# Kernel tuning notes

Hardware: AMD Instinct MI355X
Metric: run time of the kernel (lower is better)

The kernel has to match this reference:

```python
import jax, jax.numpy as jnp
import numpy as np
from jax import lax

# init kwargs (hardcoded per module config)
T_D = 0.3            # condensation radius
T_B = 0.85           # min beta threshold
FEATURE_LENGTH = 9   # x[:, FEATURE_LENGTH:] are predictions
N_TOT_FEAT = 17      # => n_ccoords = 17 - 14 = 3
MAX_COND = 1024      # static pad size for the boolean-mask gather output

B = 4
S = 250000
N = B * S


def setup_inputs() -> dict:
    key = jax.random.key(0)
    kx, = jax.random.split(key, 1)
    x = jax.random.uniform(kx, (N, N_TOT_FEAT), dtype=jnp.float32)  # betas in [0,1)
    row_splits = jnp.arange(B + 1, dtype=jnp.int32) * S             # equal ragged splits
    return {"x": x, "row_splits": row_splits}


def _condense(x, n_seg, seg_len):
    """Greedy BuildCondensates (hard/soft=False): per segment, repeatedly pick the
    unassigned point of max beta (>= T_B), assign all unassigned points within
    radius T_D of it in cluster-coordinate space, until no candidate remains."""
    n_ccoords = x.shape[-1] - 14
    x_pred = x[:, FEATURE_LENGTH:]
    betas = x_pred[:, 0].reshape(n_seg, seg_len)                     # (B,S)
    cc = x_pred[:, x_pred.shape[-1] - n_ccoords:].reshape(n_seg, seg_len, n_ccoords)
    col = jnp.arange(seg_len, dtype=jnp.int32)[None, :]              # (1,S)

    asso0 = -jnp.ones((n_seg, seg_len), jnp.int32)
    iscond0 = jnp.zeros((n_seg, seg_len), jnp.int32)

    def body(state):
        asso, iscond, _ = state
        unassigned = asso < 0
        score = jnp.where(unassigned, betas, -jnp.inf)
        max_idx = jnp.argmax(score, axis=1).astype(jnp.int32)        # (B,) per-segment argmax beta
        max_beta = jnp.take_along_axis(score, max_idx[:, None], axis=1)[:, 0]
        found = max_beta >= T_B                                      # (B,)
        c = jnp.take_along_axis(cc, max_idx[:, None, None], axis=1)  # (B,1,nc)
        distsq = jnp.sum((cc - c) ** 2, axis=-1)                     # (B,S)
        assign = unassigned & (distsq < T_D * T_D) & found[:, None]
        asso = jnp.where(assign, max_idx[:, None], asso)
        iscond = jnp.where(assign & (col == max_idx[:, None]), 1, iscond)
        return (asso, iscond, jnp.any(found))

    asso, iscond, _ = lax.while_loop(lambda s: s[2], body,
                                     (asso0, iscond0, jnp.array(True)))
    ncond_per_seg = jnp.sum(iscond, axis=1, dtype=jnp.int32)         # (B,)
    # output row splits for condensates: [0, cumsum...]
    ncond = jnp.concatenate([jnp.zeros((1,), jnp.int32),
                             jnp.cumsum(ncond_per_seg).astype(jnp.int32)])
    return asso, iscond.reshape(-1), ncond


def reference(x, row_splits):
    n_seg = row_splits.shape[0] - 1          # static
    seg_len = x.shape[0] // n_seg            # equal splits assumed (matches setup)
    _, iscond, ncond = _condense(x, n_seg, seg_len)
    # boolean-mask gather dout = x[iscond > 0], padded to static MAX_COND rows
    idx = jnp.nonzero(iscond > 0, size=MAX_COND, fill_value=0)[0]
    total = jnp.sum(iscond)
    valid = (jnp.arange(MAX_COND) < total).astype(x.dtype)           # (K,)
    dout = x[idx] * valid[:, None]                                   # (K, F), zero-padded
    return dout, ncond
```

## Files before the change

### kernel.cpp

```cpp
#include <hip/hip_runtime.h>
#include <stdint.h>

typedef unsigned long long u64;
typedef unsigned int u32;
typedef unsigned char u8;


#define DSQ(ax,ay,az,bx,by,bz) \
    __fadd_rn(__fadd_rn(__fmul_rn(__fsub_rn(ax,bx),__fsub_rn(ax,bx)), \
                        __fmul_rn(__fsub_rn(ay,by),__fsub_rn(ay,by))), \
              __fmul_rn(__fsub_rn(az,bz),__fsub_rn(az,bz)))

#define INS5(k, cx, cy, cz) do { u64 _k = (k); \
    if (_k > K5) { \
      if (_k > K4) { K5 = K4; \
        if (_k > K3) { K4 = K3; X4=X3; Y4=Y3; Z4=Z3; \
          if (_k > K2) { K3 = K2; X3=X2; Y3=Y2; Z3=Z2; \
            if (_k > K1) { K2 = K1; X2=X1; Y2=Y1; Z2=Z1; \
                           K1 = _k; X1=(cx); Y1=(cy); Z1=(cz); } \
            else { K2 = _k; X2=(cx); Y2=(cy); Z2=(cz); } } \
          else { K3 = _k; X3=(cx); Y3=(cy); Z3=(cz); } } \
        else { K4 = _k; X4=(cx); Y4=(cy); Z4=(cz); } } \
      else K5 = _k; \
    } } while (0)

__global__ void init_kernel(int* segCount, int* condTotal, int* scanned,
                            int* doneF, int* aliveCnt, int nseg) {
    int t = threadIdx.x;
    if (t < nseg) {
        segCount[t] = 0; condTotal[t] = 0; scanned[t] = 0;
        doneF[t] = 0; aliveCnt[t] = 0;
    }
}

__launch_bounds__(256)
__global__ void filter_scan0(const float* __restrict__ x, int S, int chunk, int bps,
                             int* __restrict__ segCount,
                             float4* __restrict__ A, int* __restrict__ iA,
                             u8* __restrict__ aliveB, int CAP,
                             u64* __restrict__ btK, float4* __restrict__ btC) {
    __shared__ float4 stg[1024];
    __shared__ int sgi[1024];
    __shared__ int s_cnt, s_base;
    __shared__ u64 mK[4][5];
    __shared__ float mC[4][12];
    const int b = blockIdx.x;
    const int s = b / bps, c = b % bps;
    const int tid = threadIdx.x, lane = tid & 63, wid = tid >> 6;
    int start = s * S + c * chunk;
    int end = min(start + chunk, s * S + S);
    if (tid == 0) s_cnt = 0;
    __syncthreads();
    for (int i = start + tid; i < end; i += 256) {
        float beta = x[(size_t)i * 17 + 9];
        if (beta >= 0.85f) {
            int p = atomicAdd(&s_cnt, 1);
            if (p < 1024) {
                stg[p] = make_float4(x[(size_t)i * 17 + 14], x[(size_t)i * 17 + 15],
                                     x[(size_t)i * 17 + 16], beta);
                sgi[p] = i;
            }
        }
    }
    __syncthreads();
    if (tid == 0) s_base = atomicAdd(&segCount[s], min(s_cnt, 1024));
    __syncthreads();
    int cnt = min(s_cnt, 1024);

    u64 K1=0,K2=0,K3=0,K4=0,K5=0;
    float X1=0,Y1=0,Z1=0,X2=0,Y2=0,Z2=0,X3=0,Y3=0,Z3=0,X4=0,Y4=0,Z4=0;
    for (int k = tid; k < cnt; k += 256) {
        int pos = s_base + k;
        float4 cd = stg[k];
        int gi = sgi[k];
        if (pos < CAP) {
            A[(size_t)s * CAP + pos] = cd;
            iA[(size_t)s * CAP + pos] = gi;
            aliveB[(size_t)s * CAP + pos] = 1;
            u64 key = ((u64)__float_as_uint(cd.w) << 32) | (u64)(~(u32)gi);
            INS5(key, cd.x, cd.y, cd.z);
        }
    }
    for (int off = 32; off > 0; off >>= 1) {
        u64 o1=__shfl_xor(K1,off), o2=__shfl_xor(K2,off), o3=__shfl_xor(K3,off),
            o4=__shfl_xor(K4,off), o5=__shfl_xor(K5,off);
        float a1=__shfl_xor(X1,off), b1=__shfl_xor(Y1,off), c1=__shfl_xor(Z1,off);
        float a2=__shfl_xor(X2,off), b2=__shfl_xor(Y2,off), c2=__shfl_xor(Z2,off);
        float a3=__shfl_xor(X3,off), b3=__shfl_xor(Y3,off), c3=__shfl_xor(Z3,off);
        float a4=__shfl_xor(X4,off), b4=__shfl_xor(Y4,off), c4=__shfl_xor(Z4,off);
        INS5(o1,a1,b1,c1); INS5(o2,a2,b2,c2); INS5(o3,a3,b3,c3); INS5(o4,a4,b4,c4);
        if (o5 > K5) K5 = o5;
    }
    if (lane == 0) {
        mK[wid][0]=K1; mK[wid][1]=K2; mK[wid][2]=K3; mK[wid][3]=K4; mK[wid][4]=K5;
        mC[wid][0]=X1; mC[wid][1]=Y1; mC[wid][2]=Z1; mC[wid][3]=X2; mC[wid][4]=Y2;
        mC[wid][5]=Z2; mC[wid][6]=X3; mC[wid][7]=Y3; mC[wid][8]=Z3; mC[wid][9]=X4;
        mC[wid][10]=Y4; mC[wid][11]=Z4;
    }
    __syncthreads();
    if (tid == 0) {
        for (int w = 1; w < 4; ++w) {
            INS5(mK[w][0], mC[w][0], mC[w][1], mC[w][2]);
            INS5(mK[w][1], mC[w][3], mC[w][4], mC[w][5]);
            INS5(mK[w][2], mC[w][6], mC[w][7], mC[w][8]);
            INS5(mK[w][3], mC[w][9], mC[w][10], mC[w][11]);
            if (mK[w][4] > K5) K5 = mK[w][4];
        }
        btK[(size_t)b*5+0]=K1; btK[(size_t)b*5+1]=K2; btK[(size_t)b*5+2]=K3;
        btK[(size_t)b*5+3]=K4; btK[(size_t)b*5+4]=K5;
        btC[(size_t)b*4+0]=make_float4(X1,Y1,Z1,0.f);
        btC[(size_t)b*4+1]=make_float4(X2,Y2,Z2,0.f);
        btC[(size_t)b*4+2]=make_float4(X3,Y3,Z3,0.f);
        btC[(size_t)b*4+3]=make_float4(X4,Y4,Z4,0.f);
    }
}

__launch_bounds__(256)
__global__ void scan_r(const float4* __restrict__ A, const int* __restrict__ iA,
                       const int* __restrict__ segCount, int CAP,
                       const float4* __restrict__ gctr,
                       const int* __restrict__ condTotal, const int* __restrict__ scanned,
                       const int* __restrict__ doneF, u8* __restrict__ aliveB,
                       u64* __restrict__ btK, float4* __restrict__ btC,
                       int* __restrict__ aliveCnt) {
    const int b = blockIdx.x;
    const int s = b >> 8, c = b & 255;
    const int tid = threadIdx.x, lane = tid & 63, wid = tid >> 6;
    __shared__ float4 ctrL[1024];
    __shared__ u64 mK[4][5];
    __shared__ float mC[4][12];
    __shared__ int wAl[4];
    if (doneF[s]) return;

    int n = segCount[s]; if (n > CAP) n = CAP;
    const int c0 = scanned[s], c1 = condTotal[s];
    const int nc = c1 - c0;
    for (int i = tid; i < nc; i += 256) ctrL[i] = gctr[(size_t)s * 1024 + c0 + i];
    __syncthreads();

    const int chunkC = (n + 255) >> 8;
    const int j0 = c * chunkC;
    const int j1 = min(j0 + chunkC, n);

    u64 K1=0,K2=0,K3=0,K4=0,K5=0;
    float X1=0,Y1=0,Z1=0,X2=0,Y2=0,Z2=0,X3=0,Y3=0,Z3=0,X4=0,Y4=0,Z4=0;
    int myAlive = 0;
    for (int j = j0 + tid; j < j1; j += 256) {
        if (!aliveB[(size_t)s * CAP + j]) continue;
        float4 cd = A[(size_t)s * CAP + j];
        bool live = true;
        for (int m = 0; m < nc; ++m) {
            float4 q = ctrL[m];
            if (DSQ(cd.x, cd.y, cd.z, q.x, q.y, q.z) < 0.09f) { live = false; break; }
        }
        if (!live) { aliveB[(size_t)s * CAP + j] = 0; continue; }
        ++myAlive;
        u64 key = ((u64)__float_as_uint(cd.w) << 32) | (u64)(~(u32)iA[(size_t)s * CAP + j]);
        INS5(key, cd.x, cd.y, cd.z);
    }
    for (int off = 32; off > 0; off >>= 1) {
        u64 o1=__shfl_xor(K1,off), o2=__shfl_xor(K2,off), o3=__shfl_xor(K3,off),
            o4=__shfl_xor(K4,off), o5=__shfl_xor(K5,off);
        float a1=__shfl_xor(X1,off), b1=__shfl_xor(Y1,off), c1v=__shfl_xor(Z1,off);
        float a2=__shfl_xor(X2,off), b2=__shfl_xor(Y2,off), c2v=__shfl_xor(Z2,off);
        float a3=__shfl_xor(X3,off), b3=__shfl_xor(Y3,off), c3v=__shfl_xor(Z3,off);
        float a4=__shfl_xor(X4,off), b4=__shfl_xor(Y4,off), c4v=__shfl_xor(Z4,off);
        INS5(o1,a1,b1,c1v); INS5(o2,a2,b2,c2v); INS5(o3,a3,b3,c3v); INS5(o4,a4,b4,c4v);
        if (o5 > K5) K5 = o5;
        myAlive += __shfl_xor(myAlive, off);
    }
    if (lane == 0) {
        mK[wid][0]=K1; mK[wid][1]=K2; mK[wid][2]=K3; mK[wid][3]=K4; mK[wid][4]=K5;
        mC[wid][0]=X1; mC[wid][1]=Y1; mC[wid][2]=Z1; mC[wid][3]=X2; mC[wid][4]=Y2;
        mC[wid][5]=Z2; mC[wid][6]=X3; mC[wid][7]=Y3; mC[wid][8]=Z3; mC[wid][9]=X4;
        mC[wid][10]=Y4; mC[wid][11]=Z4;
        wAl[wid] = myAlive;
    }
    __syncthreads();
    if (tid == 0) {
        for (int w = 1; w < 4; ++w) {
            INS5(mK[w][0], mC[w][0], mC[w][1], mC[w][2]);
            INS5(mK[w][1], mC[w][3], mC[w][4], mC[w][5]);
            INS5(mK[w][2], mC[w][6], mC[w][7], mC[w][8]);
            INS5(mK[w][3], mC[w][9], mC[w][10], mC[w][11]);
            if (mK[w][4] > K5) K5 = mK[w][4];
        }
        btK[(size_t)b*5+0]=K1; btK[(size_t)b*5+1]=K2; btK[(size_t)b*5+2]=K3;
        btK[(size_t)b*5+3]=K4; btK[(size_t)b*5+4]=K5;
        btC[(size_t)b*4+0]=make_float4(X1,Y1,Z1,0.f);
        btC[(size_t)b*4+1]=make_float4(X2,Y2,Z2,0.f);
        btC[(size_t)b*4+2]=make_float4(X3,Y3,Z3,0.f);
        btC[(size_t)b*4+3]=make_float4(X4,Y4,Z4,0.f);
        int tot = wAl[0] + wAl[1] + wAl[2] + wAl[3];
        if (tot) atomicAdd(&aliveCnt[s], tot);
    }
}

__launch_bounds__(64)
__global__ void pop_k(const u64* __restrict__ btK, const float4* __restrict__ btC,
                      float4* __restrict__ gctr, int* __restrict__ gctrGi,
                      int* __restrict__ condTotal, int* __restrict__ scanned,
                      int* __restrict__ doneF, int* __restrict__ aliveCnt, int check) {
    const int s = blockIdx.x, lane = threadIdx.x;
    if (doneF[s]) return;
    if (check && aliveCnt[s] == 0) { if (lane == 0) doneF[s] = 1; return; }

    u64 k[16]; float4 c[16];
    u64 h = 0;
    #pragma unroll
    for (int q = 0; q < 16; ++q) {
        int bb = (s << 8) + (lane << 2) + (q >> 2);
        int slot = q & 3;
        k[q] = btK[(size_t)bb * 5 + slot];
        c[q] = btC[(size_t)bb * 4 + slot];
        if ((q & 3) == 0) {
            u64 k5 = btK[(size_t)bb * 5 + 4];
            if (k5 > h) h = k5;
        }
    }
    for (int off = 32; off > 0; off >>= 1) {
        u64 o = __shfl_xor(h, off);
        if (o > h) h = o;
    }
    const u64 H = h;

    int ct = condTotal[s];
    const int start = ct;
    while (ct < 1024) {
        u64 mk = k[0]; float4 mc = c[0];
        #pragma unroll
        for (int q = 1; q < 16; ++q)
            if (k[q] > mk) { mk = k[q]; mc = c[q]; }
        for (int off = 32; off > 0; off >>= 1) {
            u64 ok = __shfl_xor(mk, off);
            float ox = __shfl_xor(mc.x, off);
            float oy = __shfl_xor(mc.y, off);
            float oz = __shfl_xor(mc.z, off);
            if (ok > mk) { mk = ok; mc.x = ox; mc.y = oy; mc.z = oz; }
        }
        if (mk <= H) break;
        #pragma unroll
        for (int q = 0; q < 16; ++q)
            if (k[q] && DSQ(c[q].x, c[q].y, c[q].z, mc.x, mc.y, mc.z) < 0.09f) k[q] = 0;
        if (lane == 0) {
            gctr[(size_t)s * 1024 + ct] = make_float4(mc.x, mc.y, mc.z, 0.f);
            gctrGi[(size_t)s * 1024 + ct] = (int)(~(u32)(mk & 0xFFFFFFFFull));
        }
        ct++;
    }
    if (lane == 0) { scanned[s] = start; condTotal[s] = ct; aliveCnt[s] = 0; }
}

__launch_bounds__(1024)
__global__ void fallback_k(const float4* __restrict__ A, const int* __restrict__ iA,
                           const int* __restrict__ segCount, int CAP,
                           const float4* __restrict__ gctr, int* __restrict__ gctrGi,
                           int* __restrict__ condTotalG, int* __restrict__ scannedG,
                           const int* __restrict__ doneF, u8* __restrict__ aliveB) {
    const int s = blockIdx.x, tid = threadIdx.x, lane = tid & 63, wid = tid >> 6;
    __shared__ float4 ctr[1024];
    __shared__ int ctrGi[1024];
    __shared__ u64 wk[2][16];
    __shared__ float4 wc[2][16];
    __shared__ u64 s_H;
    __shared__ int s_alive;
    if (doneF[s]) return;

    const float4* cand = A + (size_t)s * CAP;
    const int* gia = iA + (size_t)s * CAP;
    u8* alv = aliveB + (size_t)s * CAP;
    int n = segCount[s]; if (n > CAP) n = CAP;
    int condTotal = condTotalG[s];
    int scanned = scannedG[s];
    for (int i = tid; i < condTotal; i += 1024) {
        ctr[i] = gctr[(size_t)s * 1024 + i];
        ctrGi[i] = gctrGi[(size_t)s * 1024 + i];
    }
    int passes = 0, par = 0;
    __syncthreads();

    while (true) {
        if (tid == 0) { s_H = 0; s_alive = 0; }
        __syncthreads();
        u64 k1 = 0, k2 = 0, k3 = 0;
        float4 C1 = make_float4(0,0,0,0), C2 = make_float4(0,0,0,0);
        int myAlive = 0;
        for (int j = tid; j < n; j += 1024) {
            if (!alv[j]) continue;
            float4 c = cand[j];
            bool live = true;
            for (int m = scanned; m < condTotal; ++m) {
                float4 q = ctr[m];
                if (DSQ(c.x, c.y, c.z, q.x, q.y, q.z) < 0.09f) { live = false; break; }
            }
            if (!live) { alv[j] = 0; continue; }
            ++myAlive;
            u64 key = ((u64)__float_as_uint(c.w) << 32) | (u64)(~(u32)gia[j]);
            if (key > k1)      { k3 = k2; k2 = k1; C2 = C1; k1 = key; C1 = c; }
            else if (key > k2) { k3 = k2; k2 = key; C2 = c; }
            else if (key > k3) { k3 = key; }
        }
        int asum = myAlive; u64 h = k3;
        for (int off = 32; off > 0; off >>= 1) {
            asum += __shfl_down(asum, off);
            u64 o = __shfl_down(h, off);
            if (o > h) h = o;
        }
        if (lane == 0) { atomicAdd(&s_alive, asum); atomicMax(&s_H, h); }
        __syncthreads();
        if (s_alive == 0) break;
        u64 H = s_H;
        scanned = condTotal;
        while (condTotal < 1024) {
            u64 mk; float4 bc;
            if (k1 >= k2) { mk = k1; bc = C1; } else { mk = k2; bc = C2; }
            for (int off = 32; off > 0; off >>= 1) {
                u64 ok = __shfl_xor(mk, off);
                float ox = __shfl_xor(bc.x, off);
                float oy = __shfl_xor(bc.y, off);
                float oz = __shfl_xor(bc.z, off);
                if (ok > mk) { mk = ok; bc.x = ox; bc.y = oy; bc.z = oz; }
            }
            if (lane == 0) { wk[par][wid] = mk; wc[par][wid] = bc; }
            __syncthreads();
            u64 bk = 0; int bL = 0;
            #pragma unroll
            for (int w = 0; w < 16; ++w) {
                u64 kk = wk[par][w];
                if (kk > bk) { bk = kk; bL = w; }
            }
            if (bk <= H) break;
            float4 cc = wc[par][bL];
            if (k1 && DSQ(C1.x, C1.y, C1.z, cc.x, cc.y, cc.z) < 0.09f) k1 = 0;
            if (k2 && DSQ(C2.x, C2.y, C2.z, cc.x, cc.y, cc.z) < 0.09f) k2 = 0;
            if (tid == 0) { ctr[condTotal] = cc; ctrGi[condTotal] = (int)(~(u32)(bk & 0xFFFFFFFFull)); }
            condTotal++;
            par ^= 1;
        }
        __syncthreads();
        if (condTotal >= 1024 || ++passes > 128) break;
    }

    for (int i = tid; i < condTotal; i += 1024)
        gctrGi[(size_t)s * 1024 + i] = ctrGi[i];
    if (tid == 0) condTotalG[s] = condTotal;
}

__global__ void finalize_kernel(const int* __restrict__ ctrGi,
                                const int* __restrict__ condTotal,
                                int* __restrict__ sorted, int* __restrict__ prefix,
                                float* __restrict__ ncond_out, int nseg, int rows) {
    __shared__ int lst[1024];
    __shared__ int pfx[9];
    int tid = threadIdx.x;
    if (tid == 0) {
        int acc = 0; pfx[0] = 0;
        for (int s2 = 0; s2 < nseg; s2++) { acc += condTotal[s2]; pfx[s2 + 1] = acc; }
    }
    __syncthreads();
    if (tid <= nseg) { prefix[tid] = pfx[tid]; ncond_out[tid] = (float)pfx[tid]; }
    for (int s2 = 0; s2 < nseg; s2++) {
        int ns = condTotal[s2]; if (ns > 1024) ns = 1024;
        for (int i = tid; i < ns; i += blockDim.x) lst[i] = ctrGi[(size_t)s2 * 1024 + i];
        __syncthreads();
        for (int i = tid; i < ns; i += blockDim.x) {
            int v = lst[i]; int rank = 0;
            for (int j = 0; j < ns; j++) rank += (lst[j] < v);
            int pos = pfx[s2] + rank;
            if (pos < rows) sorted[pos] = v;
        }
        __syncthreads();
    }
}

__global__ void emit_kernel(const float* __restrict__ x, const int* __restrict__ sorted,
                            const int* __restrict__ prefix, float* __restrict__ out,
                            int rows, int nseg) {
    int e = blockIdx.x * blockDim.x + threadIdx.x;
    if (e >= rows * 17) return;
    int total = prefix[nseg];
    int j = e / 17, k = e - j * 17;
    float v = 0.f;
    if (j < total) v = x[(size_t)sorted[j] * 17 + k];
    out[e] = v;
}

extern "C" void kernel_launch(void* const* d_in, const int* in_sizes, int n_in,
                              void* d_out, int out_size, void* d_ws, size_t ws_size,
                              hipStream_t stream) {
    const float* x = (const float*)d_in[0];
    const int nseg = in_sizes[1] - 1;
    const int N = in_sizes[0] / 17;
    const int S = N / nseg;
    const int rows = (out_size - (nseg + 1)) / 17;
    const int NROUNDS = 2;

    const int bps = 256;
    const int nBlocks = nseg * bps;
    const int chunk = (S + bps - 1) / bps;

    size_t fixedBytes = (size_t)nseg * 1024 * 16  +
                        (size_t)nBlocks * 4 * 16  +
                        (size_t)nBlocks * 5 * 8   +
                        (size_t)nseg * 1024 * 4   +
                        (size_t)nseg * 4 * 5  +
                        (size_t)rows * 4 + (size_t)(nseg + 1) * 4 + 8192;
    size_t perCand = (size_t)nseg * (16 + 4 + 1);
    size_t avail = (ws_size > fixedBytes) ? (ws_size - fixedBytes) : 0;
    int CAP = (int)(avail / perCand);
    if (CAP > 65536) CAP = 65536;
    if (CAP < 1) CAP = 1;

    char* w = (char*)d_ws;
    float4* A    = (float4*)w;                 w += (size_t)nseg * CAP * 16;
    float4* ctr  = (float4*)w;                 w += (size_t)nseg * 1024 * 16;
    float4* btC  = (float4*)w;                 w += (size_t)nBlocks * 4 * 16;
    u64* btK     = (u64*)w;                    w += (size_t)nBlocks * 5 * 8;
    int* iA      = (int*)w;                    w += (size_t)nseg * CAP * 4;
    int* ctrGi   = (int*)w;                    w += (size_t)nseg * 1024 * 4;
    int* segCount  = (int*)w;                  w += (size_t)nseg * 4;
    int* condTotal = (int*)w;                  w += (size_t)nseg * 4;
    int* scanned   = (int*)w;                  w += (size_t)nseg * 4;
    int* doneF     = (int*)w;                  w += (size_t)nseg * 4;
    int* aliveCnt  = (int*)w;                  w += (size_t)nseg * 4;
    int* sorted    = (int*)w;                  w += (size_t)rows * 4;
    int* prefix    = (int*)w;                  w += (size_t)(nseg + 1) * 4;
    u8* aliveB     = (u8*)w;
    float* out = (float*)d_out;

    init_kernel<<<1, 64, 0, stream>>>(segCount, condTotal, scanned, doneF,
                                      aliveCnt, nseg);
    filter_scan0<<<nBlocks, 256, 0, stream>>>(x, S, chunk, bps, segCount,
                                              A, iA, aliveB, CAP, btK, btC);
    pop_k<<<nseg, 64, 0, stream>>>(btK, btC, ctr, ctrGi, condTotal, scanned,
                                   doneF, aliveCnt, 0);
    for (int r = 0; r < NROUNDS; ++r) {
        scan_r<<<nBlocks, 256, 0, stream>>>(A, iA, segCount, CAP, ctr, condTotal,
                                            scanned, doneF, aliveB, btK, btC, aliveCnt);
        pop_k<<<nseg, 64, 0, stream>>>(btK, btC, ctr, ctrGi, condTotal, scanned,
                                       doneF, aliveCnt, 1);
    }
    fallback_k<<<nseg, 1024, 0, stream>>>(A, iA, segCount, CAP, ctr, ctrGi,
                                          condTotal, scanned, doneF, aliveB);
    finalize_kernel<<<1, 256, 0, stream>>>(ctrGi, condTotal, sorted, prefix,
                                           out + (size_t)rows * 17, nseg, rows);
    emit_kernel<<<(rows * 17 + 255) / 256, 256, 0, stream>>>(x, sorted, prefix, out,
                                                             rows, nseg);
}
```

Before: 165.6 us.

## Vectorize filter loads as float4 groups of four rows, shrink pop shuffles

The filter kernel now processes four consecutive 17-float rows per thread by loading only the needed float4 words, extracting betas and cluster coordinates for each row, and reserving staging slots with one shared atomic per thread. This replaces scalar strided loads and per-row atomics. The pop kernel's argmax reduction now shuffles a source-lane index instead of three coordinates, then broadcasts the winner once. The init kernel is replaced by a memset. The change assumes S is divisible by 4 and that the input base is 16-byte aligned; each block now covers one group per thread, which relies on chunkG being at most 256.

```diff
diff --git a/kernel.cpp b/kernel.cpp
--- a/kernel.cpp
+++ b/kernel.cpp
@@ -24,17 +24,8 @@
       else K5 = _k; \
     } } while (0)
 
-__global__ void init_kernel(int* segCount, int* condTotal, int* scanned,
-                            int* doneF, int* aliveCnt, int nseg) {
-    int t = threadIdx.x;
-    if (t < nseg) {
-        segCount[t] = 0; condTotal[t] = 0; scanned[t] = 0;
-        doneF[t] = 0; aliveCnt[t] = 0;
-    }
-}
-
 __launch_bounds__(256)
-__global__ void filter_scan0(const float* __restrict__ x, int S, int chunk, int bps,
+__global__ void filter_scan0(const float* __restrict__ x, int Sg, int chunkG, int bps,
                              int* __restrict__ segCount,
                              float4* __restrict__ A, int* __restrict__ iA,
                              u8* __restrict__ aliveB, int CAP,
@@ -47,21 +38,36 @@
     const int b = blockIdx.x;
     const int s = b / bps, c = b % bps;
     const int tid = threadIdx.x, lane = tid & 63, wid = tid >> 6;
-    int start = s * S + c * chunk;
-    int end = min(start + chunk, s * S + S);
+    const int segG0 = s * Sg;
+    const int g = segG0 + c * chunkG + tid;
+    const bool valid = (g < segG0 + Sg) && (tid < chunkG);
     if (tid == 0) s_cnt = 0;
     __syncthreads();
-    for (int i = start + tid; i < end; i += 256) {
-        float beta = x[(size_t)i * 17 + 9];
-        if (beta >= 0.85f) {
-            int p = atomicAdd(&s_cnt, 1);
-            if (p < 1024) {
-                stg[p] = make_float4(x[(size_t)i * 17 + 14], x[(size_t)i * 17 + 15],
-                                     x[(size_t)i * 17 + 16], beta);
-                sgi[p] = i;
-            }
-        }
-    }
+
+    float be0=0, be1=0, be2=0, be3=0;
+    float4 cc0, cc1, cc2, cc3;
+    int r0 = 0;
+    if (valid) {
+        const float4* p = (const float4*)x + (size_t)g * 17;
+        float4 v2 = p[2],  v3 = p[3],  v4 = p[4];
+        float4 v6 = p[6],  v7 = p[7],  v8 = p[8];
+        float4 v10 = p[10], v12 = p[12];
+        float4 v15 = p[15], v16 = p[16];
+        r0 = g * 4;
+        be0 = v2.y;  cc0 = make_float4(v3.z,  v3.w,  v4.x,  be0);
+        be1 = v6.z;  cc1 = make_float4(v7.w,  v8.x,  v8.y,  be1);
+        be2 = v10.w; cc2 = make_float4(v12.x, v12.y, v12.z, be2);
+        be3 = v15.x; cc3 = make_float4(v16.y, v16.z, v16.w, be3);
+    }
+    bool h0 = valid && (be0 >= 0.85f), h1 = valid && (be1 >= 0.85f);
+    bool h2 = valid && (be2 >= 0.85f), h3 = valid && (be3 >= 0.85f);
+    int nh = (h0?1:0) + (h1?1:0) + (h2?1:0) + (h3?1:0);
+    int p0 = 0;
+    if (nh) p0 = atomicAdd(&s_cnt, nh);
+    if (h0) { if (p0 < 1024) { stg[p0] = cc0; sgi[p0] = r0;     } p0++; }
+    if (h1) { if (p0 < 1024) { stg[p0] = cc1; sgi[p0] = r0 + 1; } p0++; }
+    if (h2) { if (p0 < 1024) { stg[p0] = cc2; sgi[p0] = r0 + 2; } p0++; }
+    if (h3) { if (p0 < 1024) { stg[p0] = cc3; sgi[p0] = r0 + 3; } p0++; }
     __syncthreads();
     if (tid == 0) s_base = atomicAdd(&segCount[s], min(s_cnt, 1024));
     __syncthreads();
@@ -231,19 +237,21 @@
         #pragma unroll
         for (int q = 1; q < 16; ++q)
             if (k[q] > mk) { mk = k[q]; mc = c[q]; }
+        int src = lane;
         for (int off = 32; off > 0; off >>= 1) {
             u64 ok = __shfl_xor(mk, off);
-            float ox = __shfl_xor(mc.x, off);
-            float oy = __shfl_xor(mc.y, off);
-            float oz = __shfl_xor(mc.z, off);
-            if (ok > mk) { mk = ok; mc.x = ox; mc.y = oy; mc.z = oz; }
+            int os = __shfl_xor(src, off);
+            if (ok > mk) { mk = ok; src = os; }
         }
         if (mk <= H) break;
+        float cx = __shfl(mc.x, src);
+        float cy = __shfl(mc.y, src);
+        float cz = __shfl(mc.z, src);
         #pragma unroll
         for (int q = 0; q < 16; ++q)
-            if (k[q] && DSQ(c[q].x, c[q].y, c[q].z, mc.x, mc.y, mc.z) < 0.09f) k[q] = 0;
+            if (k[q] && DSQ(c[q].x, c[q].y, c[q].z, cx, cy, cz) < 0.09f) k[q] = 0;
         if (lane == 0) {
-            gctr[(size_t)s * 1024 + ct] = make_float4(mc.x, mc.y, mc.z, 0.f);
+            gctr[(size_t)s * 1024 + ct] = make_float4(cx, cy, cz, 0.f);
             gctrGi[(size_t)s * 1024 + ct] = (int)(~(u32)(mk & 0xFFFFFFFFull));
         }
         ct++;
@@ -397,7 +405,8 @@
 
     const int bps = 256;
     const int nBlocks = nseg * bps;
-    const int chunk = (S + bps - 1) / bps;
+    const int Sg = S >> 2;
+    const int chunkG = (Sg + bps - 1) / bps;
 
     size_t fixedBytes = (size_t)nseg * 1024 * 16  +
                         (size_t)nBlocks * 4 * 16  +
@@ -428,9 +437,8 @@
     u8* aliveB     = (u8*)w;
     float* out = (float*)d_out;
 
-    init_kernel<<<1, 64, 0, stream>>>(segCount, condTotal, scanned, doneF,
-                                      aliveCnt, nseg);
-    filter_scan0<<<nBlocks, 256, 0, stream>>>(x, S, chunk, bps, segCount,
+    hipMemsetAsync(segCount, 0, (size_t)nseg * 5 * 4, stream);
+    filter_scan0<<<nBlocks, 256, 0, stream>>>(x, Sg, chunkG, bps, segCount,
                                               A, iA, aliveB, CAP, btK, btC);
     pop_k<<<nseg, 64, 0, stream>>>(btK, btC, ctr, ctrGi, condTotal, scanned,
                                    doneF, aliveCnt, 0);
```

Result: faster. 158.0 us (-4.6%).
